# Performance work log

Measured on AMD Instinct MI355X. Metric: run time of the kernel, lower is better.

## Reference

```python
import jax, jax.numpy as jnp
import numpy as np

B, N, ADA, L, D_OUT, C_T, N_DIS = 8, 2048, 16, 64, 16, 4, 8
H = L // D_OUT  # 4 heads emulated via split/cat on the batch dim


def setup_inputs() -> dict:
    key = jax.random.key(0)
    ks = jax.random.split(key, 12)
    f = lambda i, shape, s=1.0: jax.random.normal(ks[i], shape, dtype=jnp.float32) * s
    return dict(
        c=f(0, (B, N, L)),
        c_condition=f(1, (B, C_T)),
        c_disease=f(2, (B, N_DIS)),
        state=f(3, (B, N, L)),
        emb_normal=f(4, (N, ADA)),                 # nn.Parameter embeddings_normal
        W_q1=f(5, (C_T, L), 0.1), b_q1=jnp.zeros((L,), jnp.float32),
        W_qr1=f(6, (1, L), 0.1),  b_qr1=jnp.zeros((L,), jnp.float32),
        W_q2=f(7, (L, L), 0.1),   b_q2=jnp.zeros((L,), jnp.float32),
        W_qr2=f(8, (L, L), 0.1),  b_qr2=jnp.zeros((L,), jnp.float32),
        Wp_gcn=f(9, (ADA, 2, L, L), 0.1),          # adaptive weight pool (cheb_k=2)
        bp_gcn=f(10, (ADA, L), 0.1),               # adaptive bias pool
    )


def _to_heads(t):
    # torch.cat(torch.split(t, D_OUT, dim=-1), dim=0): [B,N,H*d] -> [H*B,N,d]
    return jnp.concatenate(jnp.split(t, H, axis=-1), axis=0)


def _from_heads(t):
    # inverse: [H*B,N,d] -> [B,N,H*d]
    return jnp.concatenate(jnp.split(t, H, axis=0), axis=-1)


def _anode_gcn(x, E, Wp, bp):
    # adaptive GCN (AGCRN-style AVWGCN): supports=[I, softmax(relu(E E^T))]
    A = jax.nn.softmax(jax.nn.relu(E @ E.T), axis=1)          # [N,N]
    xg = jnp.stack([x, jnp.einsum('nm,bmc->bnc', A, x)], 1)   # [B,2,N,C]
    Wn = jnp.einsum('nd,dkio->nkio', E, Wp)                   # per-node weights
    bn = E @ bp                                               # [N,L]
    return jnp.einsum('bkni,nkio->bno', xg, Wn) + bn


def reference(c, c_condition, c_disease, state, emb_normal,
              W_q1, b_q1, W_qr1, b_qr1, W_q2, b_q2, W_qr2, b_qr2,
              Wp_gcn, bp_gcn):
    # gated query path
    Qt = jax.nn.sigmoid(c_condition[:, None, :] @ W_q1 + b_q1)        # [B,1,L]
    Qt = jnp.tanh((Qt * c) @ W_q2 + b_q2)                             # [B,N,L]
    # disease loop vectorized: sum_n sigmoid(Linear(c_disease[:, n:n+1]))
    qr = jax.nn.sigmoid(c_disease[:, :, None] * W_qr1[0] + b_qr1)     # [B,D,L]
    qr = qr.sum(axis=1, keepdims=True)                                # [B,1,L]
    qr = Qt + jnp.tanh((qr * c) @ W_qr2 + b_qr2)                      # [B,N,L]
    qr_h = _to_heads(qr)  # computed in the original but unused in output

    theta = _to_heads(state)                                          # [HB,N,d]
    ct = jnp.tanh(_anode_gcn(c, emb_normal, Wp_gcn, bp_gcn))          # [B,N,L]
    ct = _to_heads(ct)                                                # [HB,N,d]

    attn = jnp.einsum('bnd,bmd->bnm', theta, theta) / jnp.sqrt(jnp.float32(D_OUT))
    attn = jax.nn.softmax(attn, axis=-1)                              # [HB,N,N]
    x = -jnp.einsum('bnm,bmd->bnd', attn, ct)                         # [HB,N,d]
    return _from_heads(x)                                             # [B,N,L]
```

## Files before the change

### kernel.cpp

```cpp
#include <hip/hip_runtime.h>
#include <hip/hip_bf16.h>

#define NN 2048
#define BB 8
#define LL 64
#define ADA 16
#define DH 16
#define HB 32
#define KT 2048

typedef __attribute__((ext_vector_type(4))) short bf16x4;
typedef __attribute__((ext_vector_type(4))) float f32x4;
typedef __attribute__((ext_vector_type(8))) unsigned short ushort8v;
typedef _Float16 half_t;
typedef __attribute__((ext_vector_type(2))) _Float16 halfx2;
typedef __attribute__((ext_vector_type(4))) _Float16 halfx4;
typedef __attribute__((ext_vector_type(8))) _Float16 halfx8;

#if defined(__HIP_DEVICE_COMPILE__)
#if __has_builtin(__builtin_amdgcn_mfma_f32_16x16x16bf16_1k)
#define MFMA16(a, b, c) __builtin_amdgcn_mfma_f32_16x16x16bf16_1k(a, b, c, 0, 0, 0)
#elif __has_builtin(__builtin_amdgcn_mfma_f32_16x16x16_bf16)
#define MFMA16(a, b, c) __builtin_amdgcn_mfma_f32_16x16x16_bf16(a, b, c, 0, 0, 0)
#else
#error "no 16x16x16 bf16 mfma builtin on device"
#endif
#if __has_builtin(__builtin_amdgcn_mfma_f32_16x16x16f16)
#define MFMA16H(a, b, c) __builtin_amdgcn_mfma_f32_16x16x16f16(a, b, c, 0, 0, 0)
#elif __has_builtin(__builtin_amdgcn_mfma_f32_16x16x16_f16)
#define MFMA16H(a, b, c) __builtin_amdgcn_mfma_f32_16x16x16_f16(a, b, c, 0, 0, 0)
#else
#error "no 16x16x16 f16 mfma builtin on device"
#endif
#if __has_builtin(__builtin_amdgcn_exp2f)
#define EXP2F(x) __builtin_amdgcn_exp2f(x)
#else
#define EXP2F(x) exp2f(x)
#endif
#else
#define MFMA16(a, b, c) (c)
#define MFMA16H(a, b, c) (c)
#define EXP2F(x) exp2f(x)
#endif

__device__ inline halfx2 cvt_pk2(float a, float b) {
#if defined(__HIP_DEVICE_COMPILE__) && __has_builtin(__builtin_amdgcn_cvt_pkrtz)
  auto r = __builtin_amdgcn_cvt_pkrtz(a, b);
  return __builtin_bit_cast(halfx2, r);
#else
  halfx2 r;
  r[0] = (_Float16)a;
  r[1] = (_Float16)b;
  return r;
#endif
}

__device__ inline unsigned short f2bf(float x) {
  __hip_bfloat16 h = __float2bfloat16(x);
  return *reinterpret_cast<unsigned short*>(&h);
}
__device__ inline float tanh_fast(float v) {
  return 1.f - 2.f / (__expf(2.f * v) + 1.f);
}

__global__ __launch_bounds__(256) void k_preps(const float* __restrict__ E,
                                               const float* __restrict__ c,
                                               const float* __restrict__ state,
                                               const float* __restrict__ Wp,
                                               unsigned short* __restrict__ A16,
                                               unsigned short* __restrict__ cT16,
                                               half_t* __restrict__ WpT,
                                               half_t* __restrict__ th16h,
                                               half_t* __restrict__ thq16h) {
  __shared__ float sbuf[4 * 2304];
  const int id = blockIdx.x;
  const int t = threadIdx.x;
  if (id < 512) {
    float(*row)[NN] = (float(*)[NN])sbuf;
    float(*red)[256] = (float(*)[256])(sbuf + 4 * NN);
    const int n = id * 4;
    float4 e[4][4];
#pragma unroll
    for (int r = 0; r < 4; ++r) {
      const float4* Er = (const float4*)(E + (size_t)(n + r) * ADA);
#pragma unroll
      for (int j = 0; j < 4; ++j) e[r][j] = Er[j];
    }
    float l[4] = {0.f, 0.f, 0.f, 0.f};
    for (int m = t; m < NN; m += 256) {
      const float4* Em = (const float4*)(E + (size_t)m * ADA);
      float4 ev[4];
#pragma unroll
      for (int j = 0; j < 4; ++j) ev[j] = Em[j];
#pragma unroll
      for (int r = 0; r < 4; ++r) {
        float s = 0.f;
#pragma unroll
        for (int j = 0; j < 4; ++j) {
          s = fmaf(e[r][j].x, ev[j].x, s);
          s = fmaf(e[r][j].y, ev[j].y, s);
          s = fmaf(e[r][j].z, ev[j].z, s);
          s = fmaf(e[r][j].w, ev[j].w, s);
        }
        float p = __expf(fmaxf(s, 0.f) - 20.f);
        row[r][m] = p;
        l[r] += p;
      }
    }
#pragma unroll
    for (int r = 0; r < 4; ++r) red[r][t] = l[r];
    __syncthreads();
    for (int off = 128; off > 0; off >>= 1) {
      if (t < off) {
#pragma unroll
        for (int r = 0; r < 4; ++r) red[r][t] += red[r][t + off];
      }
      __syncthreads();
    }
    float inv[4];
#pragma unroll
    for (int r = 0; r < 4; ++r) inv[r] = 1.f / red[r][0];
    for (int m = t; m < NN; m += 256) {
#pragma unroll
      for (int r = 0; r < 4; ++r)
        A16[(size_t)(n + r) * NN + m] = f2bf(row[r][m] * inv[r]);
    }
  } else if (id < 768) {
    float(*ld)[68] = (float(*)[68])sbuf;
    const int idx = id - 512;
    const int m0 = (idx & 31) * 64;
    const int b = idx >> 5;
    {
      const int r = t & 63, cq = t >> 6;
      const float* cp = c + ((size_t)b * NN + m0 + r) * LL + cq * 16;
#pragma unroll
      for (int u = 0; u < 4; ++u)
        *(float4*)&ld[r][cq * 16 + 4 * u] = *(const float4*)(cp + 4 * u);
    }
    __syncthreads();
    const int o = t & 63, mq = t >> 6;
    unsigned short outv[16];
#pragma unroll
    for (int v = 0; v < 16; ++v) outv[v] = f2bf(ld[mq * 16 + v][o]);
    unsigned short* op = cT16 + ((size_t)b * LL + o) * NN + m0 + mq * 16;
    *(ushort8v*)op = *(const ushort8v*)&outv[0];
    *(ushort8v*)(op + 8) = *(const ushort8v*)&outv[8];
  } else if (id < 800) {
    float(*ld)[68] = (float(*)[68])sbuf;
    const int k0 = (id - 768) * 64;
    {
      const int r = t & 63, cq = t >> 6;
      const float* wp = Wp + (size_t)(k0 + r) * LL + cq * 16;
#pragma unroll
      for (int u = 0; u < 4; ++u)
        *(float4*)&ld[r][cq * 16 + 4 * u] = *(const float4*)(wp + 4 * u);
    }
    __syncthreads();
    const int o = t & 63, kq = t >> 6;
    halfx8 h0, h1;
#pragma unroll
    for (int v = 0; v < 8; ++v) {
      h0[v] = (half_t)ld[kq * 16 + v][o];
      h1[v] = (half_t)ld[kq * 16 + 8 + v][o];
    }
    half_t* op = WpT + (size_t)o * KT + k0 + kq * 16;
    *(halfx8*)op = h0;
    *(halfx8*)(op + 8) = h1;
  } else {
    const int idx = id - 800;
    const int n0 = (idx & 31) * 64;
    const int b = idx >> 5;
    const int r = t >> 2, h = t & 3;
    const float QS = 0.25f * 1.4426950408889634f;
    const float* sp = state + ((size_t)b * NN + n0 + r) * LL + h * DH;
    half_t tk[16], tq[16];
#pragma unroll
    for (int u = 0; u < 4; ++u) {
      float4 sv = *(const float4*)(sp + 4 * u);
      tk[4 * u + 0] = (half_t)sv.x; tk[4 * u + 1] = (half_t)sv.y;
      tk[4 * u + 2] = (half_t)sv.z; tk[4 * u + 3] = (half_t)sv.w;
      tq[4 * u + 0] = (half_t)(QS * sv.x); tq[4 * u + 1] = (half_t)(QS * sv.y);
      tq[4 * u + 2] = (half_t)(QS * sv.z); tq[4 * u + 3] = (half_t)(QS * sv.w);
    }
    const size_t base = ((size_t)(h * 8 + b) * NN + n0 + r) * DH;
    *(halfx8*)(th16h + base) = *(const halfx8*)&tk[0];
    *(halfx8*)(th16h + base + 8) = *(const halfx8*)&tk[8];
    *(halfx8*)(thq16h + base) = *(const halfx8*)&tq[0];
    *(halfx8*)(thq16h + base + 8) = *(const halfx8*)&tq[8];
  }
}

__global__ __launch_bounds__(256) void k_gemm1(const unsigned short* __restrict__ A16,
                                               const unsigned short* __restrict__ cT16,
                                               float* __restrict__ cg0,
                                               float* __restrict__ cg1) {
  __shared__ unsigned short sA[64][72];
  __shared__ unsigned short sB[64][72];
  const int t = threadIdx.x;
  const int n0 = blockIdx.x * 64;
  const int b = blockIdx.y;
  const int kh = blockIdx.z;
  const int wv = t >> 6, lane = t & 63;
  const int lr = lane & 15, lg = lane >> 4;
  const unsigned short* cb = cT16 + (size_t)b * LL * NN;
  const int sr = t >> 2, sc = (t & 3) * 16;
  f32x4 acc[4];
#pragma unroll
  for (int ot = 0; ot < 4; ++ot) acc[ot] = (f32x4){0.f, 0.f, 0.f, 0.f};

  for (int k0 = kh * (NN / 2); k0 < (kh + 1) * (NN / 2); k0 += 64) {
    __syncthreads();
    {
      const unsigned short* ga = A16 + (size_t)(n0 + sr) * NN + k0 + sc;
      *(ushort8v*)&sA[sr][sc] = *(const ushort8v*)ga;
      *(ushort8v*)&sA[sr][sc + 8] = *(const ushort8v*)(ga + 8);
      const unsigned short* gb = cb + (size_t)sr * NN + k0 + sc;
      *(ushort8v*)&sB[sr][sc] = *(const ushort8v*)gb;
      *(ushort8v*)&sB[sr][sc + 8] = *(const ushort8v*)(gb + 8);
    }
    __syncthreads();
#pragma unroll
    for (int ks = 0; ks < 4; ++ks) {
      bf16x4 a = *(const bf16x4*)&sA[16 * wv + lr][ks * 16 + 4 * lg];
#pragma unroll
      for (int ot = 0; ot < 4; ++ot) {
        bf16x4 bq = *(const bf16x4*)&sB[ot * 16 + lr][ks * 16 + 4 * lg];
        acc[ot] = MFMA16(a, bq, acc[ot]);
      }
    }
  }
  float* outp = (kh ? cg1 : cg0) + ((size_t)b * NN + n0 + 16 * wv) * LL;
#pragma unroll
  for (int ot = 0; ot < 4; ++ot)
#pragma unroll
    for (int reg = 0; reg < 4; ++reg)
      outp[(size_t)(4 * lg + reg) * LL + ot * 16 + lr] = acc[ot][reg];
}

__global__ __launch_bounds__(256) void k_gcn4(const float* __restrict__ E,
                                              const half_t* __restrict__ WpT,
                                              const float* __restrict__ bp,
                                              const float* __restrict__ c,
                                              const float* __restrict__ cg0,
                                              const float* __restrict__ cg1,
                                              half_t* __restrict__ vt16h) {
  __shared__ half_t sW[32][136];
  __shared__ float sE[64][17];
  __shared__ float sbp[16][32];
  const int t = threadIdx.x;
  const int n0 = blockIdx.x * 64;
  const int b = blockIdx.y;
  const int oh = blockIdx.z;
  const int wv = t >> 6, lane = t & 63;
  const int lr = lane & 15, lg = lane >> 4;
  {
    const int r = t >> 2, dq = (t & 3) * 4;
    float4 ev = *(const float4*)(E + (size_t)(n0 + r) * ADA + dq);
    sE[r][dq + 0] = ev.x; sE[r][dq + 1] = ev.y;
    sE[r][dq + 2] = ev.z; sE[r][dq + 3] = ev.w;
    const int d = t >> 4, o2 = (t & 15) * 2;
    float2 bv = *(const float2*)(bp + d * LL + oh * 32 + o2);
    sbp[d][o2] = bv.x;
    sbp[d][o2 + 1] = bv.y;
  }
  float xr[8][4];
  {
    const size_t rbase = ((size_t)b * NN + n0 + 16 * wv + lr) * LL;
#pragma unroll
    for (int q = 0; q < 4; ++q) {
      float4 v = *(const float4*)(c + rbase + q * 16 + 4 * lg);
      xr[q][0] = v.x; xr[q][1] = v.y; xr[q][2] = v.z; xr[q][3] = v.w;
    }
#pragma unroll
    for (int q = 0; q < 4; ++q) {
      float4 a = *(const float4*)(cg0 + rbase + q * 16 + 4 * lg);
      float4 b2 = *(const float4*)(cg1 + rbase + q * 16 + 4 * lg);
      xr[4 + q][0] = a.x + b2.x; xr[4 + q][1] = a.y + b2.y;
      xr[4 + q][2] = a.z + b2.z; xr[4 + q][3] = a.w + b2.w;
    }
  }
  __syncthreads();
  f32x4 acc[2];
#pragma unroll
  for (int ot2 = 0; ot2 < 2; ++ot2) {
    f32x4 s = (f32x4){0.f, 0.f, 0.f, 0.f};
#pragma unroll
    for (int d = 0; d < ADA; ++d) {
      const float bpv = sbp[d][ot2 * 16 + lr];
#pragma unroll
      for (int reg = 0; reg < 4; ++reg)
        s[reg] = fmaf(sE[16 * wv + 4 * lg + reg][d], bpv, s[reg]);
    }
    acc[ot2] = s;
  }
  const int so = t >> 3, sq = t & 7;
  halfx8 wreg[2];
  {
    const half_t* p = WpT + (size_t)(oh * 32 + so) * KT + sq * 16;
    wreg[0] = *(const halfx8*)p;
    wreg[1] = *(const halfx8*)(p + 8);
  }
  for (int dd = 0; dd < ADA; ++dd) {
    __syncthreads();
    *(halfx8*)&sW[so][sq * 16] = wreg[0];
    *(halfx8*)&sW[so][sq * 16 + 8] = wreg[1];
    __syncthreads();
    if (dd < ADA - 1) {
      const half_t* p = WpT + (size_t)(oh * 32 + so) * KT + (dd + 1) * 128 + sq * 16;
      wreg[0] = *(const halfx8*)p;
      wreg[1] = *(const halfx8*)(p + 8);
    }
    const float e = sE[16 * wv + lr][dd];
    halfx4 af[8];
#pragma unroll
    for (int kt = 0; kt < 8; ++kt)
#pragma unroll
      for (int j = 0; j < 4; ++j) af[kt][j] = (half_t)(e * xr[kt][j]);
#pragma unroll
    for (int kt = 0; kt < 8; ++kt) {
#pragma unroll
      for (int ot2 = 0; ot2 < 2; ++ot2) {
        halfx4 bq = *(const halfx4*)&sW[ot2 * 16 + lr][kt * 16 + 4 * lg];
        acc[ot2] = MFMA16H(af[kt], bq, acc[ot2]);
      }
    }
  }
#pragma unroll
  for (int ot2 = 0; ot2 < 2; ++ot2) {
    const int h = oh * 2 + ot2;
    halfx4 o4;
#pragma unroll
    for (int reg = 0; reg < 4; ++reg) o4[reg] = (half_t)tanh_fast(acc[ot2][reg]);
    *(halfx4*)(vt16h + ((size_t)(h * 8 + b) * DH + lr) * NN + n0 + 16 * wv + 4 * lg) = o4;
  }
}

__global__ __launch_bounds__(512, 4) void k_attn5(const half_t* __restrict__ th16h,
                                                  const half_t* __restrict__ thq16h,
                                                  const half_t* __restrict__ vt16h,
                                                  float* __restrict__ out) {
  __shared__ float sred[8][8][16][16];
  float* dfl = &sred[0][0][0][0];
  const int hb = blockIdx.x;
  const int h = hb >> 3, b = hb & 7;
  const int wv = threadIdx.x >> 6, lane = threadIdx.x & 63;
  const int q0 = blockIdx.y * 128;
  const int lr = lane & 15, lg = lane >> 4;
  const half_t* th = th16h + (size_t)hb * NN * DH;
  const half_t* thq = thq16h + (size_t)hb * NN * DH;
  const half_t* vrow = vt16h + ((size_t)hb * DH + lr) * NN;
  halfx4 qf[8];
#pragma unroll
  for (int f = 0; f < 8; ++f)
    qf[f] = *(const halfx4*)(thq + (size_t)(q0 + 16 * f + lr) * DH + 4 * lg);
  const float SH = 8.f * 1.4426950408889634f;
  const f32x4 shiftv = {-SH, -SH, -SH, -SH};
  f32x4 acc[8];
  float den[8];
#pragma unroll
  for (int f = 0; f < 8; ++f) { acc[f] = (f32x4){0.f, 0.f, 0.f, 0.f}; den[f] = 0.f; }

  const int mb = wv * (NN / 8);
  halfx4 kf = *(const halfx4*)(th + (size_t)(mb + lr) * DH + 4 * lg);
  halfx4 vf = *(const halfx4*)(vrow + mb + 4 * lg);
  for (int mt = 0; mt < NN / 128; ++mt) {
    halfx4 kf_n = kf, vf_n = vf;
    if (mt < NN / 128 - 1) {
      const int mn = mb + (mt + 1) * 16;
      kf_n = *(const halfx4*)(th + (size_t)(mn + lr) * DH + 4 * lg);
      vf_n = *(const halfx4*)(vrow + mn + 4 * lg);
    }
#pragma unroll
    for (int f = 0; f < 8; ++f) {
      f32x4 s = MFMA16H(kf, qf[f], shiftv);
      float p0 = EXP2F(s[0]), p1 = EXP2F(s[1]), p2 = EXP2F(s[2]), p3 = EXP2F(s[3]);
      den[f] += (p0 + p1) + (p2 + p3);
      halfx2 lo = cvt_pk2(p0, p1), hi = cvt_pk2(p2, p3);
      halfx4 pf;
      pf[0] = lo[0]; pf[1] = lo[1]; pf[2] = hi[0]; pf[3] = hi[1];
      acc[f] = MFMA16H(pf, vf, acc[f]);
    }
    kf = kf_n; vf = vf_n;
  }
#pragma unroll
  for (int f = 0; f < 8; ++f) {
    den[f] += __shfl_xor(den[f], 16);
    den[f] += __shfl_xor(den[f], 32);
  }
  if (lane < 16) {
#pragma unroll
    for (int f = 0; f < 8; ++f) dfl[(wv * 8 + f) * 16 + lane] = den[f];
  }
  __syncthreads();
  const int t = threadIdx.x;
  const int fo = t >> 6, ro = (t >> 2) & 15, duo = (t & 3) * 4;
  float ds = 0.f;
#pragma unroll
  for (int w = 0; w < 8; ++w) ds += dfl[(w * 8 + fo) * 16 + ro];
  __syncthreads();
#pragma unroll
  for (int f = 0; f < 8; ++f) {
#pragma unroll
    for (int reg = 0; reg < 4; ++reg) sred[wv][f][4 * lg + reg][lr] = acc[f][reg];
  }
  __syncthreads();
  float4 ns = make_float4(0.f, 0.f, 0.f, 0.f);
#pragma unroll
  for (int w = 0; w < 8; ++w) {
    float4 v = *(const float4*)&sred[w][fo][ro][duo];
    ns.x += v.x; ns.y += v.y; ns.z += v.z; ns.w += v.w;
  }
  const float inv = -1.f / ds;
  float4 o = make_float4(ns.x * inv, ns.y * inv, ns.z * inv, ns.w * inv);
  *(float4*)(out + ((size_t)b * NN + q0 + 16 * fo + ro) * LL + h * DH + duo) = o;
}

extern "C" void kernel_launch(void* const* d_in, const int* in_sizes, int n_in,
                              void* d_out, int out_size, void* d_ws, size_t ws_size,
                              hipStream_t stream) {
  const float* c = (const float*)d_in[0];
  const float* state = (const float*)d_in[3];
  const float* E = (const float*)d_in[4];
  const float* Wp = (const float*)d_in[13];
  const float* bp = (const float*)d_in[14];
  float* out = (float*)d_out;

  unsigned short* A16 = (unsigned short*)d_ws;
  unsigned short* cT16 = A16 + (size_t)NN * NN;
  half_t* WpT = (half_t*)(cT16 + (size_t)BB * LL * NN);
  float* cg0 = (float*)(WpT + (size_t)LL * KT);
  float* cg1 = cg0 + (size_t)BB * NN * LL;
  half_t* th16h = (half_t*)(cg1 + (size_t)BB * NN * LL);
  half_t* thq16h = th16h + (size_t)HB * NN * DH;
  half_t* vt16h = thq16h + (size_t)HB * NN * DH;

  k_preps<<<1056, 256, 0, stream>>>(E, c, state, Wp, A16, cT16, WpT, th16h, thq16h);
  k_gemm1<<<dim3(NN / 64, BB, 2), 256, 0, stream>>>(A16, cT16, cg0, cg1);
  k_gcn4<<<dim3(NN / 64, BB, 2), 256, 0, stream>>>(E, WpT, bp, c, cg0, cg1, vt16h);
  k_attn5<<<dim3(HB, NN / 128), 512, 0, stream>>>(th16h, thq16h, vt16h, out);
}
```

Before: 72.78 us.

## Fuse graph-propagation GEMM into GCN kernel and drop split-K intermediates

Merges the A·c GEMM kernel and the per-node GCN kernel into one kernel. The full-K GEMM result stays in shared memory instead of going through two fp32 global buffers (split-K halves). Each block now also computes all four heads' output columns instead of two. This removes a kernel launch and the global round-trip of cg0/cg1, and avoids reading A16 twice. In exchange the grid shrinks from 512 to 256 blocks, each running a longer serial K loop, and shared memory is reused between phases.

```diff
diff --git a/kernel.cpp b/kernel.cpp
--- a/kernel.cpp
+++ b/kernel.cpp
@@ -190,67 +190,23 @@
   }
 }
 
-__global__ __launch_bounds__(256) void k_gemm1(const unsigned short* __restrict__ A16,
-                                               const unsigned short* __restrict__ cT16,
-                                               float* __restrict__ cg0,
-                                               float* __restrict__ cg1) {
-  __shared__ unsigned short sA[64][72];
-  __shared__ unsigned short sB[64][72];
+__global__ __launch_bounds__(256) void k_gcnf(const unsigned short* __restrict__ A16,
+                                              const unsigned short* __restrict__ cT16,
+                                              const float* __restrict__ E,
+                                              const half_t* __restrict__ WpT,
+                                              const float* __restrict__ bp,
+                                              const float* __restrict__ c,
+                                              half_t* __restrict__ vt16h) {
+  __shared__ __align__(16) char smemU[36864];
+  __shared__ float sE[64][17];
+  __shared__ float sbp[16][64];
+  unsigned short(*sA)[72] = (unsigned short(*)[72])smemU;
+  unsigned short(*sB)[72] = (unsigned short(*)[72])(smemU + 18432);
+  float(*cgs)[68] = (float(*)[68])smemU;
+  half_t(*sW)[136] = (half_t(*)[136])smemU;
   const int t = threadIdx.x;
   const int n0 = blockIdx.x * 64;
   const int b = blockIdx.y;
-  const int kh = blockIdx.z;
-  const int wv = t >> 6, lane = t & 63;
-  const int lr = lane & 15, lg = lane >> 4;
-  const unsigned short* cb = cT16 + (size_t)b * LL * NN;
-  const int sr = t >> 2, sc = (t & 3) * 16;
-  f32x4 acc[4];
-#pragma unroll
-  for (int ot = 0; ot < 4; ++ot) acc[ot] = (f32x4){0.f, 0.f, 0.f, 0.f};
-
-  for (int k0 = kh * (NN / 2); k0 < (kh + 1) * (NN / 2); k0 += 64) {
-    __syncthreads();
-    {
-      const unsigned short* ga = A16 + (size_t)(n0 + sr) * NN + k0 + sc;
-      *(ushort8v*)&sA[sr][sc] = *(const ushort8v*)ga;
-      *(ushort8v*)&sA[sr][sc + 8] = *(const ushort8v*)(ga + 8);
-      const unsigned short* gb = cb + (size_t)sr * NN + k0 + sc;
-      *(ushort8v*)&sB[sr][sc] = *(const ushort8v*)gb;
-      *(ushort8v*)&sB[sr][sc + 8] = *(const ushort8v*)(gb + 8);
-    }
-    __syncthreads();
-#pragma unroll
-    for (int ks = 0; ks < 4; ++ks) {
-      bf16x4 a = *(const bf16x4*)&sA[16 * wv + lr][ks * 16 + 4 * lg];
-#pragma unroll
-      for (int ot = 0; ot < 4; ++ot) {
-        bf16x4 bq = *(const bf16x4*)&sB[ot * 16 + lr][ks * 16 + 4 * lg];
-        acc[ot] = MFMA16(a, bq, acc[ot]);
-      }
-    }
-  }
-  float* outp = (kh ? cg1 : cg0) + ((size_t)b * NN + n0 + 16 * wv) * LL;
-#pragma unroll
-  for (int ot = 0; ot < 4; ++ot)
-#pragma unroll
-    for (int reg = 0; reg < 4; ++reg)
-      outp[(size_t)(4 * lg + reg) * LL + ot * 16 + lr] = acc[ot][reg];
-}
-
-__global__ __launch_bounds__(256) void k_gcn4(const float* __restrict__ E,
-                                              const half_t* __restrict__ WpT,
-                                              const float* __restrict__ bp,
-                                              const float* __restrict__ c,
-                                              const float* __restrict__ cg0,
-                                              const float* __restrict__ cg1,
-                                              half_t* __restrict__ vt16h) {
-  __shared__ half_t sW[32][136];
-  __shared__ float sE[64][17];
-  __shared__ float sbp[16][32];
-  const int t = threadIdx.x;
-  const int n0 = blockIdx.x * 64;
-  const int b = blockIdx.y;
-  const int oh = blockIdx.z;
   const int wv = t >> 6, lane = t & 63;
   const int lr = lane & 15, lg = lane >> 4;
   {
@@ -258,10 +214,8 @@
     float4 ev = *(const float4*)(E + (size_t)(n0 + r) * ADA + dq);
     sE[r][dq + 0] = ev.x; sE[r][dq + 1] = ev.y;
     sE[r][dq + 2] = ev.z; sE[r][dq + 3] = ev.w;
-    const int d = t >> 4, o2 = (t & 15) * 2;
-    float2 bv = *(const float2*)(bp + d * LL + oh * 32 + o2);
-    sbp[d][o2] = bv.x;
-    sbp[d][o2 + 1] = bv.y;
+    const int bi = t * 4;
+    *(float4*)&sbp[bi >> 6][bi & 63] = *(const float4*)(bp + bi);
   }
   float xr[8][4];
   {
@@ -271,44 +225,75 @@
       float4 v = *(const float4*)(c + rbase + q * 16 + 4 * lg);
       xr[q][0] = v.x; xr[q][1] = v.y; xr[q][2] = v.z; xr[q][3] = v.w;
     }
-#pragma unroll
-    for (int q = 0; q < 4; ++q) {
-      float4 a = *(const float4*)(cg0 + rbase + q * 16 + 4 * lg);
-      float4 b2 = *(const float4*)(cg1 + rbase + q * 16 + 4 * lg);
-      xr[4 + q][0] = a.x + b2.x; xr[4 + q][1] = a.y + b2.y;
-      xr[4 + q][2] = a.z + b2.z; xr[4 + q][3] = a.w + b2.w;
-    }
-  }
-  __syncthreads();
-  f32x4 acc[2];
-#pragma unroll
-  for (int ot2 = 0; ot2 < 2; ++ot2) {
+  }
+  const unsigned short* cb = cT16 + (size_t)b * LL * NN;
+  const int sr = t >> 2, sc2 = (t & 3) * 16;
+  f32x4 gacc[4];
+#pragma unroll
+  for (int ot = 0; ot < 4; ++ot) gacc[ot] = (f32x4){0.f, 0.f, 0.f, 0.f};
+  for (int k0 = 0; k0 < NN; k0 += 64) {
+    __syncthreads();
+    {
+      const unsigned short* ga = A16 + (size_t)(n0 + sr) * NN + k0 + sc2;
+      *(ushort8v*)&sA[sr][sc2] = *(const ushort8v*)ga;
+      *(ushort8v*)&sA[sr][sc2 + 8] = *(const ushort8v*)(ga + 8);
+      const unsigned short* gb = cb + (size_t)sr * NN + k0 + sc2;
+      *(ushort8v*)&sB[sr][sc2] = *(const ushort8v*)gb;
+      *(ushort8v*)&sB[sr][sc2 + 8] = *(const ushort8v*)(gb + 8);
+    }
+    __syncthreads();
+#pragma unroll
+    for (int ks = 0; ks < 4; ++ks) {
+      bf16x4 a = *(const bf16x4*)&sA[16 * wv + lr][ks * 16 + 4 * lg];
+#pragma unroll
+      for (int ot = 0; ot < 4; ++ot) {
+        bf16x4 bq = *(const bf16x4*)&sB[ot * 16 + lr][ks * 16 + 4 * lg];
+        gacc[ot] = MFMA16(a, bq, gacc[ot]);
+      }
+    }
+  }
+  __syncthreads();
+#pragma unroll
+  for (int ot = 0; ot < 4; ++ot)
+#pragma unroll
+    for (int reg = 0; reg < 4; ++reg)
+      cgs[16 * wv + 4 * lg + reg][ot * 16 + lr] = gacc[ot][reg];
+  __syncthreads();
+#pragma unroll
+  for (int q = 0; q < 4; ++q) {
+    float4 v = *(const float4*)&cgs[16 * wv + lr][q * 16 + 4 * lg];
+    xr[4 + q][0] = v.x; xr[4 + q][1] = v.y; xr[4 + q][2] = v.z; xr[4 + q][3] = v.w;
+  }
+  __syncthreads();
+  f32x4 acc[4];
+#pragma unroll
+  for (int ot = 0; ot < 4; ++ot) {
     f32x4 s = (f32x4){0.f, 0.f, 0.f, 0.f};
 #pragma unroll
     for (int d = 0; d < ADA; ++d) {
-      const float bpv = sbp[d][ot2 * 16 + lr];
+      const float bpv = sbp[d][ot * 16 + lr];
 #pragma unroll
       for (int reg = 0; reg < 4; ++reg)
         s[reg] = fmaf(sE[16 * wv + 4 * lg + reg][d], bpv, s[reg]);
     }
-    acc[ot2] = s;
-  }
-  const int so = t >> 3, sq = t & 7;
-  halfx8 wreg[2];
+    acc[ot] = s;
+  }
+  const int so = t >> 2, sq = t & 3;
+  halfx8 wreg[4];
   {
-    const half_t* p = WpT + (size_t)(oh * 32 + so) * KT + sq * 16;
-    wreg[0] = *(const halfx8*)p;
-    wreg[1] = *(const halfx8*)(p + 8);
+    const half_t* p = WpT + (size_t)so * KT;
+#pragma unroll
+    for (int u = 0; u < 4; ++u) wreg[u] = *(const halfx8*)(p + (sq + 4 * u) * 8);
   }
   for (int dd = 0; dd < ADA; ++dd) {
     __syncthreads();
-    *(halfx8*)&sW[so][sq * 16] = wreg[0];
-    *(halfx8*)&sW[so][sq * 16 + 8] = wreg[1];
+#pragma unroll
+    for (int u = 0; u < 4; ++u) *(halfx8*)&sW[so][(sq + 4 * u) * 8] = wreg[u];
     __syncthreads();
     if (dd < ADA - 1) {
-      const half_t* p = WpT + (size_t)(oh * 32 + so) * KT + (dd + 1) * 128 + sq * 16;
-      wreg[0] = *(const halfx8*)p;
-      wreg[1] = *(const halfx8*)(p + 8);
+      const half_t* p = WpT + (size_t)so * KT + (size_t)(dd + 1) * 128;
+#pragma unroll
+      for (int u = 0; u < 4; ++u) wreg[u] = *(const halfx8*)(p + (sq + 4 * u) * 8);
     }
     const float e = sE[16 * wv + lr][dd];
     halfx4 af[8];
@@ -319,19 +304,18 @@
 #pragma unroll
     for (int kt = 0; kt < 8; ++kt) {
 #pragma unroll
-      for (int ot2 = 0; ot2 < 2; ++ot2) {
-        halfx4 bq = *(const halfx4*)&sW[ot2 * 16 + lr][kt * 16 + 4 * lg];
-        acc[ot2] = MFMA16H(af[kt], bq, acc[ot2]);
+      for (int ot = 0; ot < 4; ++ot) {
+        halfx4 bq = *(const halfx4*)&sW[ot * 16 + lr][kt * 16 + 4 * lg];
+        acc[ot] = MFMA16H(af[kt], bq, acc[ot]);
       }
     }
   }
 #pragma unroll
-  for (int ot2 = 0; ot2 < 2; ++ot2) {
-    const int h = oh * 2 + ot2;
+  for (int ot = 0; ot < 4; ++ot) {
     halfx4 o4;
 #pragma unroll
-    for (int reg = 0; reg < 4; ++reg) o4[reg] = (half_t)tanh_fast(acc[ot2][reg]);
-    *(halfx4*)(vt16h + ((size_t)(h * 8 + b) * DH + lr) * NN + n0 + 16 * wv + 4 * lg) = o4;
+    for (int reg = 0; reg < 4; ++reg) o4[reg] = (half_t)tanh_fast(acc[ot][reg]);
+    *(halfx4*)(vt16h + ((size_t)(ot * 8 + b) * DH + lr) * NN + n0 + 16 * wv + 4 * lg) = o4;
   }
 }
 
@@ -428,14 +412,11 @@
   unsigned short* A16 = (unsigned short*)d_ws;
   unsigned short* cT16 = A16 + (size_t)NN * NN;
   half_t* WpT = (half_t*)(cT16 + (size_t)BB * LL * NN);
-  float* cg0 = (float*)(WpT + (size_t)LL * KT);
-  float* cg1 = cg0 + (size_t)BB * NN * LL;
-  half_t* th16h = (half_t*)(cg1 + (size_t)BB * NN * LL);
+  half_t* th16h = WpT + (size_t)LL * KT;
   half_t* thq16h = th16h + (size_t)HB * NN * DH;
   half_t* vt16h = thq16h + (size_t)HB * NN * DH;
 
   k_preps<<<1056, 256, 0, stream>>>(E, c, state, Wp, A16, cT16, WpT, th16h, thq16h);
-  k_gemm1<<<dim3(NN / 64, BB, 2), 256, 0, stream>>>(A16, cT16, cg0, cg1);
-  k_gcn4<<<dim3(NN / 64, BB, 2), 256, 0, stream>>>(E, WpT, bp, c, cg0, cg1, vt16h);
+  k_gcnf<<<dim3(NN / 64, BB), 256, 0, stream>>>(A16, cT16, E, WpT, bp, c, vt16h);
   k_attn5<<<dim3(HB, NN / 128), 512, 0, stream>>>(th16h, thq16h, vt16h, out);
 }
```

After: 85.24 us. +17.1%, slower.
